# Optimization experiments

Hardware: AMD Instinct MI355X
Metric: run time of the kernel (lower is better)

The kernel has to match this reference:

```python
import jax, jax.numpy as jnp
import numpy as np

N_NODES = 50000
N_EDGES = 1000000
IN_C = 128
HID_C = 128
N_REL = 8


def rgcn_conv(x, W, root, b, src, dst, et, n_rel):
    # PyG-style RGCNConv: per-relation linear transform of source features,
    # mean-aggregated per (target node, relation), plus root transform + bias.
    n = x.shape[0]
    h = jnp.einsum('nd,rdh->nrh', x, W)          # [N, R, H] per-relation transforms
    msgs = h[src, et]                            # [E, H] gather per-edge message
    seg = dst * n_rel + et                       # combined (node, relation) segment id
    agg = jax.ops.segment_sum(msgs, seg, num_segments=n * n_rel)        # [N*R, H]
    cnt = jax.ops.segment_sum(jnp.ones_like(msgs[:, 0]), seg, num_segments=n * n_rel)
    agg = agg / jnp.maximum(cnt, 1.0)[:, None]   # mean over edges of each relation
    return agg.reshape(n, n_rel, -1).sum(axis=1) + x @ root + b


def setup_inputs() -> dict:
    key = jax.random.key(0)
    ks = jax.random.split(key, 12)
    s = 1.0 / np.sqrt(IN_C)
    sh = 1.0 / np.sqrt(HID_C)
    return {
        'x': jax.random.normal(ks[0], (N_NODES, IN_C), dtype=jnp.float32),
        'ei': jax.random.randint(ks[1], (2, N_EDGES), 0, N_NODES, dtype=jnp.int32),
        'et': jax.random.randint(ks[2], (N_EDGES,), 0, N_REL, dtype=jnp.int32),
        'W1': jax.random.normal(ks[3], (N_REL, IN_C, HID_C), dtype=jnp.float32) * s,
        'root1': jax.random.normal(ks[4], (IN_C, HID_C), dtype=jnp.float32) * s,
        'b1': jnp.zeros((HID_C,), dtype=jnp.float32),
        'W2': jax.random.normal(ks[5], (N_REL, HID_C, HID_C), dtype=jnp.float32) * sh,
        'root2': jax.random.normal(ks[6], (HID_C, HID_C), dtype=jnp.float32) * sh,
        'b2': jnp.zeros((HID_C,), dtype=jnp.float32),
        'lin_W': jax.random.normal(ks[7], (HID_C, HID_C), dtype=jnp.float32) * sh,
        'lin_b': jnp.zeros((HID_C,), dtype=jnp.float32),
    }


def reference(x, ei, et, W1, root1, b1, W2, root2, b2, lin_W, lin_b):
    src, dst = ei[0], ei[1]
    h = jax.nn.relu(rgcn_conv(x, W1, root1, b1, src, dst, et, N_REL))
    h = rgcn_conv(h, W2, root2, b2, src, dst, et, N_REL)
    return h @ lin_W + lin_b
```

## Files before the change

kernel.cpp:

```cpp
#include <hip/hip_runtime.h>
#include <hip/hip_bf16.h>

#define N_NODES 50000
#define N_EDGES 1000000
#define C       128
#define N_REL   8
#define N_SEG   (N_NODES * N_REL)
#define KTOT    (N_REL * C + C)
#define KC_CNT  (KTOT / 32)
#define A_STRIDE 1160
#define NCHUNK  ((N_SEG + 1023) / 1024)
#define MV_N    (N_SEG + 1 + N_EDGES)
#define MROW    32
#define NBLK    ((N_NODES + MROW - 1) / MROW)
#define FE_BLK  ((N_EDGES + 511) / 512)

typedef __hip_bfloat16  bf16;
typedef __hip_bfloat162 bf162;
typedef __attribute__((ext_vector_type(8))) short short8;
typedef __attribute__((ext_vector_type(4))) float f32x4;
typedef __attribute__((ext_vector_type(2))) float f32x2;

__device__ __forceinline__ size_t frag_index(int k, int n) {
    int nt = n >> 4, n15 = n & 15;
    int kc = k >> 5, quad = (k >> 3) & 3, j = k & 7;
    int lane = quad * 16 + n15;
    return ((size_t)(nt * KC_CNT + kc) * 64 + lane) * 8 + j;
}

#define CVT_BLOCKS ((N_NODES * C / 2) / 256)
#define CNT_BLOCKS ((N_EDGES + 255) / 256)
__global__ void prep_kernel(const float2* __restrict__ xf, unsigned int* __restrict__ xb,
                            const int* __restrict__ dst, const int* __restrict__ et,
                            int* __restrict__ cnt, int* __restrict__ rank) {
    int bid = blockIdx.x;
    if (bid < CVT_BLOCKS) {
        int i = bid * 256 + threadIdx.x;
        float2 v = xf[i];
        union { bf162 h; unsigned int u; } cv;
        cv.h = bf162(__float2bfloat16(v.x), __float2bfloat16(v.y));
        xb[i] = cv.u;
    } else {
        int e = (bid - CVT_BLOCKS) * 256 + threadIdx.x;
        if (e < N_EDGES) rank[e] = atomicAdd(&cnt[dst[e] * N_REL + et[e]], 1);
    }
}

#define RP_B  (KTOT * C / 256)
#define RPT_B ((KTOT / 16) * (C / 16))
__global__ void scanA_kernel(const int* __restrict__ cnt, int* __restrict__ offs,
                             int* __restrict__ partials,
                             const float* __restrict__ W1, const float* __restrict__ root1,
                             const float* __restrict__ W2, const float* __restrict__ root2,
                             const float* __restrict__ linW,
                             const float* __restrict__ b2, const float* __restrict__ linb,
                             bf16* __restrict__ Bp1, bf16* __restrict__ Bp2,
                             float* __restrict__ b2p) {
    int bid = blockIdx.x;
    int t   = threadIdx.x;
    if (bid < NCHUNK) {
        __shared__ int tot[256];
        int base = bid * 1024 + t * 4;
        int v0 = (base + 0 < N_SEG) ? cnt[base + 0] : 0;
        int v1 = (base + 1 < N_SEG) ? cnt[base + 1] : 0;
        int v2 = (base + 2 < N_SEG) ? cnt[base + 2] : 0;
        int v3 = (base + 3 < N_SEG) ? cnt[base + 3] : 0;
        int tsum = v0 + v1 + v2 + v3;
        tot[t] = tsum;
        __syncthreads();
        for (int d = 1; d < 256; d <<= 1) {
            int x = tot[t];
            int y = (t >= d) ? tot[t - d] : 0;
            __syncthreads();
            tot[t] = x + y;
            __syncthreads();
        }
        int excl = tot[t] - tsum;
        if (base + 0 < N_SEG) offs[base + 0] = excl;
        if (base + 1 < N_SEG) offs[base + 1] = excl + v0;
        if (base + 2 < N_SEG) offs[base + 2] = excl + v0 + v1;
        if (base + 3 < N_SEG) offs[base + 3] = excl + v0 + v1 + v2;
        if (t == 255) partials[bid] = tot[255];
    } else if (bid < NCHUNK + RP_B) {
        int idx = (bid - NCHUNK) * 256 + t;
        int k = idx >> 7, n = idx & 127;
        float val;
        if (k < N_REL * C) val = W1[(size_t)k * C + n];
        else               val = root1[(size_t)(k - N_REL * C) * C + n];
        Bp1[frag_index(k, n)] = __float2bfloat16(val);
    } else if (bid < NCHUNK + RP_B + RPT_B) {
        __shared__ float Wt[16][128];
        __shared__ float Lt[128][16];
        int tileid = bid - NCHUNK - RP_B;
        int kt = tileid >> 3;
        int n0 = (tileid & 7) * 16;
        int k0 = kt * 16;
        const float* baseW = (k0 < N_REL * C) ? (W2 + (size_t)k0 * C)
                                              : (root2 + (size_t)(k0 - N_REL * C) * C);
#pragma unroll
        for (int r = 0; r < 8; r++) {
            int idx = t + r * 256;
            Wt[idx >> 7][idx & 127] = baseW[idx];
        }
#pragma unroll
        for (int r = 0; r < 8; r++) {
            int idx = t + r * 256;
            Lt[idx >> 4][idx & 15] = linW[(size_t)(idx >> 4) * C + n0 + (idx & 15)];
        }
        __syncthreads();
        int ty = t >> 4, tx = t & 15;
        float acc = 0.f;
#pragma unroll 8
        for (int m = 0; m < 128; m++)
            acc += Wt[ty][m] * Lt[m][tx];
        Bp2[frag_index(k0 + ty, n0 + tx)] = __float2bfloat16(acc);
    } else {
        if (t < 128) {
            float acc = linb[t];
            for (int m = 0; m < C; m++)
                acc += b2[m] * linW[(size_t)m * C + t];
            b2p[t] = acc;
        }
    }
}

__global__ void fillB_kernel(const int* __restrict__ src, const int* __restrict__ dst,
                             const int* __restrict__ et,
                             const int* __restrict__ offs_raw,
                             const int* __restrict__ partials,
                             int* __restrict__ offs_final,
                             const int* __restrict__ rank,
                             int* __restrict__ srcs_out) {
    __shared__ int s[512];
    int t = threadIdx.x;
    int bid = blockIdx.x;
    s[t] = (t < NCHUNK) ? partials[t] : 0;
    __syncthreads();
    for (int d = 1; d < 512; d <<= 1) {
        int x = s[t];
        int y = (t >= d) ? s[t - d] : 0;
        __syncthreads();
        s[t] = x + y;
        __syncthreads();
    }
    if (bid < NCHUNK) {
        int add = (bid == 0) ? 0 : s[bid - 1];
        int base = bid * 1024 + t * 2;
#pragma unroll
        for (int j = 0; j < 2; j++) {
            int idx = base + j;
            if (idx < N_SEG) offs_final[idx] = offs_raw[idx] + add;
        }
        if (bid == 0 && t == 0) offs_final[N_SEG] = N_EDGES;
    } else {
        int e = (bid - NCHUNK) * 512 + t;
        if (e < N_EDGES) {
            int seg = dst[e] * N_REL + et[e];
            int chunk = seg >> 10;
            int base = offs_raw[seg] + ((chunk == 0) ? 0 : s[chunk - 1]);
            srcs_out[base + rank[e]] = src[e];
        }
    }
}

template <int RELU, int OUT_F32, int COPY_CSR>
__global__ __launch_bounds__(512, 4) void fused_layer(
        const unsigned int* __restrict__ featu,
        const int*   __restrict__ offs,
        const int*   __restrict__ srcs,
        const short8* __restrict__ Bp,
        const float* __restrict__ bias,
        void* __restrict__ outp,
        int* __restrict__ offs2, int* __restrict__ srcs2)
{
    __shared__ __align__(16) unsigned int At[MROW * (A_STRIDE / 2)];
    const int tid  = threadIdx.x;
    const int lane = tid & 63;
    const int w    = tid >> 6;
    const int v0   = blockIdx.x * MROW;

    if (tid < 4 * MROW) At[(tid >> 2) * (A_STRIDE / 2) + 576 + (tid & 3)] = 0u;

    if (COPY_CSR) {
        for (int i = blockIdx.x * 512 + tid; i < MV_N; i += NBLK * 512) {
            if (i < N_SEG + 1) offs2[i] = offs[i];
            else               srcs2[i - (N_SEG + 1)] = srcs[i - (N_SEG + 1)];
        }
    }

    for (int q = tid; q < MROW * 64; q += 512) {
        int node = q >> 6, pch = q & 63;
        unsigned int sval = 0u;
        if (v0 + node < N_NODES) sval = featu[(size_t)(v0 + node) * 64 + pch];
        At[node * (A_STRIDE / 2) + 512 + pch] = sval;
    }

    {
        const int segLo   = w * 32;
        const int segBase = v0 * 8 + segLo;
        int oidx = segBase + ((lane < 32) ? lane : 32);
        if (oidx > N_SEG) oidx = N_SEG;
        const int offsReg = offs[oidx];
#define OFFS(L) __builtin_amdgcn_readlane(offsReg, (L))

        int curSeg = segLo;
        int i      = OFFS(0);
        int segBeg = i;
        int segEnd = OFFS(1);
        const int eend = OFFS(32);
        f32x2 acc2 = {0.f, 0.f};

        auto FLUSH = [&](int upto) {
            while (segEnd == upto) {
                float inv = (segEnd > segBeg) ? 1.0f / (float)(segEnd - segBeg) : 0.0f;
                union { bf162 h; unsigned int u; } cv;
                cv.h = bf162(__float2bfloat16(acc2.x * inv), __float2bfloat16(acc2.y * inv));
                At[(curSeg >> 3) * (A_STRIDE / 2) + (curSeg & 7) * 64 + lane] = cv.u;
                acc2.x = 0.f; acc2.y = 0.f;
                segBeg = segEnd;
                curSeg++;
                segEnd = OFFS(curSeg + 1 - segLo);
            }
        };
        auto LOADF = [&](unsigned int (&v)[16], int base) {
            int sv[16];
#pragma unroll
            for (int j = 0; j < 16; j++) sv[j] = srcs[base + j];
#pragma unroll
            for (int j = 0; j < 16; j++) v[j] = featu[(size_t)sv[j] * 64 + lane];
        };
        auto FOLD16 = [&](unsigned int (&v)[16]) {
#pragma unroll
            for (int j = 0; j < 16; j++) {
                FLUSH(i + j);
                union { unsigned int u; float f; } lo, hi;
                lo.u = v[j] << 16;
                hi.u = v[j] & 0xFFFF0000u;
                f32x2 tadd = {lo.f, hi.f};
                acc2 += tadd;
            }
            i += 16;
        };

        unsigned int valsA[16], valsB[16];
        const int nfull = (eend - i) >> 4;
        if (nfull > 0) {
            LOADF(valsA, i);
            int b = 0;
            while (true) {
                if (b + 1 < nfull) LOADF(valsB, i + 16);
                FOLD16(valsA);
                b++;
                if (b >= nfull) break;
                if (b + 1 < nfull) LOADF(valsA, i + 16);
                FOLD16(valsB);
                b++;
                if (b >= nfull) break;
            }
        }
        {
            const int m = eend - i;
            if (m > 0) {
                int sv[16];
#pragma unroll
                for (int j = 0; j < 16; j++) if (j < m) sv[j] = srcs[i + j];
#pragma unroll
                for (int j = 0; j < 16; j++) if (j < m) valsA[j] = featu[(size_t)sv[j] * 64 + lane];
#pragma unroll
                for (int j = 0; j < 16; j++) {
                    if (j < m) {
                        FLUSH(i + j);
                        union { unsigned int u; float f; } lo, hi;
                        lo.u = valsA[j] << 16;
                        hi.u = valsA[j] & 0xFFFF0000u;
                        f32x2 tadd = {lo.f, hi.f};
                        acc2 += tadd;
                    }
                }
            }
        }
        while (curSeg < segLo + 32) {
            float inv = (segEnd > segBeg) ? 1.0f / (float)(segEnd - segBeg) : 0.0f;
            union { bf162 h; unsigned int u; } cv;
            cv.h = bf162(__float2bfloat16(acc2.x * inv), __float2bfloat16(acc2.y * inv));
            At[(curSeg >> 3) * (A_STRIDE / 2) + (curSeg & 7) * 64 + lane] = cv.u;
            acc2.x = 0.f; acc2.y = 0.f;
            segBeg = segEnd;
            curSeg++;
            if (curSeg < segLo + 32)
                segEnd = OFFS(curSeg + 1 - segLo);
        }
#undef OFFS
    }
    __syncthreads();

    const int quad = lane >> 4, n15 = lane & 15;
    f32x4 acc0 = {0.f, 0.f, 0.f, 0.f};
    f32x4 acc1 = {0.f, 0.f, 0.f, 0.f};
    const short* Ash = (const short*)At;
    const short8* BpW = Bp + (size_t)w * KC_CNT * 64;

    short8 b0 = BpW[0 * 64 + lane];
    short8 b1 = BpW[1 * 64 + lane];
    short8 b2 = BpW[2 * 64 + lane];
    short8 b3 = BpW[3 * 64 + lane];
#pragma unroll
    for (int kc = 0; kc < KC_CNT; kc += 4) {
        short8 cb[4] = {b0, b1, b2, b3};
        if (kc + 4 < KC_CNT) {
            b0 = BpW[(kc + 4) * 64 + lane];
            b1 = BpW[(kc + 5) * 64 + lane];
            b2 = BpW[(kc + 6) * 64 + lane];
            b3 = BpW[(kc + 7) * 64 + lane];
        }
#pragma unroll
        for (int u = 0; u < 4; u++) {
            const short* abase = Ash + (kc + u) * 32 + quad * 8;
            short8 a0 = *reinterpret_cast<const short8*>(abase + n15 * A_STRIDE);
            short8 a1 = *reinterpret_cast<const short8*>(abase + (n15 + 16) * A_STRIDE);
            acc0 = __builtin_amdgcn_mfma_f32_16x16x32_bf16(a0, cb[u], acc0, 0, 0, 0);
            acc1 = __builtin_amdgcn_mfma_f32_16x16x32_bf16(a1, cb[u], acc1, 0, 0, 0);
        }
    }

    {
        int col = w * 16 + n15;
        float bv = bias[col];
#pragma unroll
        for (int r = 0; r < 4; r++) {
            int m = quad * 4 + r;
            float v = acc0[r] + bv;
            if (RELU) v = fmaxf(v, 0.f);
            if (OUT_F32) ((float*)outp)[(size_t)(v0 + m) * C + col] = v;
            else         ((bf16*)outp)[(size_t)(v0 + m) * C + col] = __float2bfloat16(v);
            int m2 = v0 + 16 + m;
            if (m2 < N_NODES) {
                float v2 = acc1[r] + bv;
                if (RELU) v2 = fmaxf(v2, 0.f);
                if (OUT_F32) ((float*)outp)[(size_t)m2 * C + col] = v2;
                else         ((bf16*)outp)[(size_t)m2 * C + col] = __float2bfloat16(v2);
            }
        }
    }
}

extern "C" void kernel_launch(void* const* d_in, const int* in_sizes, int n_in,
                              void* d_out, int out_size, void* d_ws, size_t ws_size,
                              hipStream_t stream) {
    const float* x     = (const float*)d_in[0];
    const int*   ei    = (const int*)d_in[1];
    const int*   et    = (const int*)d_in[2];
    const float* W1    = (const float*)d_in[3];
    const float* root1 = (const float*)d_in[4];
    const float* b1    = (const float*)d_in[5];
    const float* W2    = (const float*)d_in[6];
    const float* root2 = (const float*)d_in[7];
    const float* b2    = (const float*)d_in[8];
    const float* linW  = (const float*)d_in[9];
    const float* linb  = (const float*)d_in[10];
    const int* src = ei;
    const int* dst = ei + N_EDGES;

    char* ob = (char*)d_out;
    int* cnt_i    = (int*)(ob + 0);
    int* offs_f   = (int*)(ob + 0);
    int* offs_t   = (int*)(ob + 1600256);
    int* partials = (int*)(ob + 3200256);
    int* srcs_t   = (int*)(ob + 3202048);
    int* rank     = (int*)(ob + 7202048);
    unsigned int* xb16 = (unsigned int*)(ob + 11202048);

    char* eb = (char*)d_in[1];
    int* offs2 = (int*)(eb + 0);
    int* srcs2 = (int*)(eb + 1600256);

    char* xbuf = (char*)d_in[0];
    unsigned int* h1 = (unsigned int*)xbuf;
    bf16*  Bp1 = (bf16*)(xbuf + 13000192);
    bf16*  Bp2 = (bf16*)(xbuf + 13295360);
    float* b2p = (float*)(xbuf + 13590528);

    float* out = (float*)d_out;

    hipMemsetAsync(cnt_i, 0, 1600000, stream);
    prep_kernel<<<CVT_BLOCKS + CNT_BLOCKS, 256, 0, stream>>>(
        (const float2*)x, xb16, dst, et, cnt_i, rank);
    scanA_kernel<<<NCHUNK + RP_B + RPT_B + 1, 256, 0, stream>>>(
        cnt_i, offs_t, partials, W1, root1, W2, root2, linW, b2, linb,
        Bp1, Bp2, b2p);
    fillB_kernel<<<NCHUNK + FE_BLK, 512, 0, stream>>>(
        src, dst, et, offs_t, partials, offs_f, rank, srcs_t);

    fused_layer<1, 0, 1><<<NBLK, 512, 0, stream>>>(
        xb16, offs_f, srcs_t, (const short8*)Bp1, b1, (void*)h1, offs2, srcs2);
    fused_layer<0, 1, 0><<<NBLK, 512, 0, stream>>>(
        h1, offs2, srcs2, (const short8*)Bp2, b2p, (void*)out, nullptr, nullptr);

    (void)in_sizes; (void)n_in; (void)out_size; (void)d_ws; (void)ws_size;
}
```

Baseline: 310.9 us.

## Deepen gather prefetch to three buffers and remap MFMA tiles per wave

The edge-gather loop now rotates three 16-entry register buffers, keeping two batches of feature loads in flight instead of one, to hide gather latency. The per-node GEMM epilogue is remapped so each wave owns 16 rows and 32 columns instead of 32 rows and 16 columns. Each wave now loads one A fragment from LDS per k-step but streams two B fragments from global memory. It also raises wave priority with s_setprio during the MFMA loop. The deeper prefetch costs more VGPRs and may lower occupancy, and the remap doubles B-fragment global traffic per wave.

```diff
diff --git a/kernel.cpp b/kernel.cpp
--- a/kernel.cpp
+++ b/kernel.cpp
@@ -242,20 +242,22 @@
             i += 16;
         };
 
-        unsigned int valsA[16], valsB[16];
+        unsigned int vA[16], vB[16], vC[16];
         const int nfull = (eend - i) >> 4;
         if (nfull > 0) {
-            LOADF(valsA, i);
+            LOADF(vA, i);
+            if (nfull > 1) LOADF(vB, i + 16);
             int b = 0;
             while (true) {
-                if (b + 1 < nfull) LOADF(valsB, i + 16);
-                FOLD16(valsA);
-                b++;
-                if (b >= nfull) break;
-                if (b + 1 < nfull) LOADF(valsA, i + 16);
-                FOLD16(valsB);
-                b++;
-                if (b >= nfull) break;
+                if (b + 2 < nfull) LOADF(vC, i + 32);
+                FOLD16(vA);
+                b++; if (b >= nfull) break;
+                if (b + 2 < nfull) LOADF(vA, i + 32);
+                FOLD16(vB);
+                b++; if (b >= nfull) break;
+                if (b + 2 < nfull) LOADF(vB, i + 32);
+                FOLD16(vC);
+                b++; if (b >= nfull) break;
             }
         }
         {
@@ -265,14 +267,14 @@
 #pragma unroll
                 for (int j = 0; j < 16; j++) if (j < m) sv[j] = srcs[i + j];
 #pragma unroll
-                for (int j = 0; j < 16; j++) if (j < m) valsA[j] = featu[(size_t)sv[j] * 64 + lane];
+                for (int j = 0; j < 16; j++) if (j < m) vA[j] = featu[(size_t)sv[j] * 64 + lane];
 #pragma unroll
                 for (int j = 0; j < 16; j++) {
                     if (j < m) {
                         FLUSH(i + j);
                         union { unsigned int u; float f; } lo, hi;
-                        lo.u = valsA[j] << 16;
-                        hi.u = valsA[j] & 0xFFFF0000u;
+                        lo.u = vA[j] << 16;
+                        hi.u = vA[j] & 0xFFFF0000u;
                         f32x2 tadd = {lo.f, hi.f};
                         acc2 += tadd;
                     }
@@ -295,50 +297,50 @@
     __syncthreads();
 
     const int quad = lane >> 4, n15 = lane & 15;
+    const int wh = w >> 2;
+    const int wc = w & 3;
     f32x4 acc0 = {0.f, 0.f, 0.f, 0.f};
     f32x4 acc1 = {0.f, 0.f, 0.f, 0.f};
     const short* Ash = (const short*)At;
-    const short8* BpW = Bp + (size_t)w * KC_CNT * 64;
-
-    short8 b0 = BpW[0 * 64 + lane];
-    short8 b1 = BpW[1 * 64 + lane];
-    short8 b2 = BpW[2 * 64 + lane];
-    short8 b3 = BpW[3 * 64 + lane];
-#pragma unroll
-    for (int kc = 0; kc < KC_CNT; kc += 4) {
-        short8 cb[4] = {b0, b1, b2, b3};
-        if (kc + 4 < KC_CNT) {
-            b0 = BpW[(kc + 4) * 64 + lane];
-            b1 = BpW[(kc + 5) * 64 + lane];
-            b2 = BpW[(kc + 6) * 64 + lane];
-            b3 = BpW[(kc + 7) * 64 + lane];
-        }
-#pragma unroll
-        for (int u = 0; u < 4; u++) {
-            const short* abase = Ash + (kc + u) * 32 + quad * 8;
-            short8 a0 = *reinterpret_cast<const short8*>(abase + n15 * A_STRIDE);
-            short8 a1 = *reinterpret_cast<const short8*>(abase + (n15 + 16) * A_STRIDE);
-            acc0 = __builtin_amdgcn_mfma_f32_16x16x32_bf16(a0, cb[u], acc0, 0, 0, 0);
-            acc1 = __builtin_amdgcn_mfma_f32_16x16x32_bf16(a1, cb[u], acc1, 0, 0, 0);
-        }
-    }
+    const short8* BpT0 = Bp + (size_t)(2 * wc)     * KC_CNT * 64;
+    const short8* BpT1 = Bp + (size_t)(2 * wc + 1) * KC_CNT * 64;
+    const short* arow = Ash + (n15 + 16 * wh) * A_STRIDE + quad * 8;
+
+    short8 b0 = BpT0[lane];
+    short8 b1 = BpT1[lane];
+    __builtin_amdgcn_s_setprio(1);
+#pragma unroll 4
+    for (int kc = 0; kc < KC_CNT; kc++) {
+        short8 cb0 = b0, cb1 = b1;
+        if (kc + 1 < KC_CNT) {
+            b0 = BpT0[(kc + 1) * 64 + lane];
+            b1 = BpT1[(kc + 1) * 64 + lane];
+        }
+        short8 a = *reinterpret_cast<const short8*>(arow + kc * 32);
+        acc0 = __builtin_amdgcn_mfma_f32_16x16x32_bf16(a, cb0, acc0, 0, 0, 0);
+        acc1 = __builtin_amdgcn_mfma_f32_16x16x32_bf16(a, cb1, acc1, 0, 0, 0);
+    }
+    __builtin_amdgcn_s_setprio(0);
 
     {
-        int col = w * 16 + n15;
-        float bv = bias[col];
+        int col0 = wc * 32 + n15;
+        int col1 = col0 + 16;
+        float bv0 = bias[col0], bv1 = bias[col1];
+        int nodeBase = v0 + wh * 16 + quad * 4;
 #pragma unroll
         for (int r = 0; r < 4; r++) {
-            int m = quad * 4 + r;
-            float v = acc0[r] + bv;
-            if (RELU) v = fmaxf(v, 0.f);
-            if (OUT_F32) ((float*)outp)[(size_t)(v0 + m) * C + col] = v;
-            else         ((bf16*)outp)[(size_t)(v0 + m) * C + col] = __float2bfloat16(v);
-            int m2 = v0 + 16 + m;
-            if (m2 < N_NODES) {
-                float v2 = acc1[r] + bv;
-                if (RELU) v2 = fmaxf(v2, 0.f);
-                if (OUT_F32) ((float*)outp)[(size_t)m2 * C + col] = v2;
-                else         ((bf16*)outp)[(size_t)m2 * C + col] = __float2bfloat16(v2);
+            int node = nodeBase + r;
+            if (node < N_NODES) {
+                float va = acc0[r] + bv0;
+                float vb = acc1[r] + bv1;
+                if (RELU) { va = fmaxf(va, 0.f); vb = fmaxf(vb, 0.f); }
+                if (OUT_F32) {
+                    ((float*)outp)[(size_t)node * C + col0] = va;
+                    ((float*)outp)[(size_t)node * C + col1] = vb;
+                } else {
+                    ((bf16*)outp)[(size_t)node * C + col0] = __float2bfloat16(va);
+                    ((bf16*)outp)[(size_t)node * C + col1] = __float2bfloat16(vb);
+                }
             }
         }
     }
```

Result: slower. 349.5 us (+12.4%).
